# Performance work log

Measured on AMD Instinct MI355X. Metric: run time of the kernel, lower is better.

## Reference

```python
import jax, jax.numpy as jnp
import numpy as np

D_MODEL = 1024
N_HEADS = 16
HEAD_DIM = 64


def setup_inputs() -> dict:
    key = jax.random.key(0)
    ks = jax.random.split(key, 9)
    B, T, C = 4, 2048, D_MODEL
    s = 1.0 / np.sqrt(C)
    return {
        "x": jax.random.normal(ks[0], (B, T, C), jnp.float32),
        "wq": jax.random.normal(ks[1], (C, C), jnp.float32) * s,
        "bq": jnp.zeros((C,), jnp.float32),
        "wk": jax.random.normal(ks[2], (C, C), jnp.float32) * s,
        "bk": jnp.zeros((C,), jnp.float32),
        "wv": jax.random.normal(ks[3], (C, C), jnp.float32) * s,
        "bv": jnp.zeros((C,), jnp.float32),
        "wo": jax.random.normal(ks[4], (C, C), jnp.float32) * s,
        "bo": jnp.zeros((C,), jnp.float32),
    }


def reference(x, wq, bq, wk, bk, wv, bv, wo, bo):
    B, T, C = x.shape
    H, Dh = N_HEADS, HEAD_DIM
    # projections -> (B, H, T, Dh)
    def split_heads(t):
        return t.reshape(B, T, H, Dh).transpose(0, 2, 1, 3)
    q = split_heads(x @ wq + bq)
    k = split_heads(x @ wk + bk)
    v = split_heads(x @ wv + bv)
    scale = 1.0 / jnp.sqrt(jnp.asarray(Dh, x.dtype))
    scores = jnp.einsum("bhqd,bhkd->bhqk", q, k) * scale  # (B,H,T,T)
    causal = jnp.tril(jnp.ones((T, T), bool))
    scores = jnp.where(causal, scores, jnp.asarray(-jnp.inf, x.dtype))
    attn = jax.nn.softmax(scores, axis=-1)
    out = jnp.einsum("bhqk,bhkd->bhqd", attn, v)
    out = out.transpose(0, 2, 1, 3).reshape(B, T, C)
    return out @ wo + bo
```

## Files before the change

kernel.cpp:

```cpp
#include <hip/hip_runtime.h>
#include <hip/hip_bf16.h>
#include <stdint.h>

#define D_MODEL 1024
#define NHEADS 16
#define HDIM 64
#define BATCH 4
#define SEQ 2048
#define M_ROWS (BATCH*SEQ)
#define BHTD ((size_t)BATCH*NHEADS*SEQ*HDIM)

typedef __attribute__((ext_vector_type(8))) short bf16x8;
typedef __attribute__((ext_vector_type(4))) float f32x4;
typedef __attribute__((ext_vector_type(16))) float f32x16;
typedef __attribute__((address_space(1))) uint32_t as1_u32;
typedef __attribute__((address_space(3))) uint32_t as3_u32;

__device__ __forceinline__ void gload_lds16(const void* g, void* l) {
    __builtin_amdgcn_global_load_lds((const as1_u32*)(uintptr_t)g,
                                     (as3_u32*)(uintptr_t)l, 16, 0, 0);
}

__device__ __forceinline__ short f2bf(float f) {
    __hip_bfloat16 h = __float2bfloat16(f);
    return *reinterpret_cast<short*>(&h);
}

__device__ __forceinline__ uint32_t cvtpk_bf16(float lo, float hi) {
    uint32_t r;
    asm("v_cvt_pk_bf16_f32 %0, %1, %2" : "=v"(r) : "v"(lo), "v"(hi));
    return r;
}

__device__ __forceinline__ float fexp2(float x) {
    return __builtin_amdgcn_exp2f(x);
}

__global__ void f32_to_bf16_k(const float* __restrict__ in, short* __restrict__ out, int n) {
    int i = (blockIdx.x * blockDim.x + threadIdx.x) * 4;
    if (i >= n) return;
    float4 v = *(const float4*)&in[i];
    short4 r;
    r.x = f2bf(v.x); r.y = f2bf(v.y); r.z = f2bf(v.z); r.w = f2bf(v.w);
    *(short4*)&out[i] = r;
}

__global__ void transpose_pack_k(const float* __restrict__ wq, const float* __restrict__ wk,
                                 const float* __restrict__ wv, const float* __restrict__ wo,
                                 short* __restrict__ qkvT, short* __restrict__ woT) {
    __shared__ float tile[32][33];
    int z = blockIdx.z;
    const float* src = (z == 0) ? wq : (z == 1) ? wk : (z == 2) ? wv : wo;
    short* dst = (z < 3) ? (qkvT + (size_t)z * D_MODEL * D_MODEL) : woT;
    int bx = blockIdx.x, by = blockIdx.y;
    int tx = threadIdx.x, ty = threadIdx.y;
#pragma unroll
    for (int r = 0; r < 32; r += 8)
        tile[ty + r][tx] = src[(size_t)(by * 32 + ty + r) * D_MODEL + bx * 32 + tx];
    __syncthreads();
#pragma unroll
    for (int r = 0; r < 32; r += 8)
        dst[(size_t)(bx * 32 + ty + r) * D_MODEL + by * 32 + tx] = f2bf(tile[tx][ty + r]);
}

template <int MODE>
__global__ __launch_bounds__(256, 2) void gemm128(const short* __restrict__ A,
                                                  const short* __restrict__ Bt,
                                                  const float* __restrict__ b0,
                                                  const float* __restrict__ b1,
                                                  const float* __restrict__ b2,
                                                  short* __restrict__ outb,
                                                  float* __restrict__ outf,
                                                  int K) {
    __shared__ short As[2][128 * 64];
    __shared__ short Bs[2][128 * 64];
    int tid = threadIdx.x;
    int lane = tid & 63, wid = tid >> 6;
    int wr = wid >> 1, wc = wid & 1;
    int lr = lane & 15, lg = lane >> 4;
    int mb = blockIdx.x * 128;
    int nb = blockIdx.y * 128;
    int srow = tid >> 3, kseg = tid & 7;

    f32x4 acc[4][4] = {};
    int nk = K / 64;

    auto STAGE = [&](int bufi, int kb) {
#pragma unroll
        for (int si = 0; si < 4; ++si) {
            int row = srow + si * 32;
            int sp = kseg ^ (row & 7);
            gload_lds16(A + (size_t)(mb + row) * K + kb + sp * 8, &As[bufi][row * 64 + kseg * 8]);
            gload_lds16(Bt + (size_t)(nb + row) * K + kb + sp * 8, &Bs[bufi][row * 64 + kseg * 8]);
        }
    };

    STAGE(0, 0);
    for (int kt = 0; kt < nk; ++kt) {
        int buf = kt & 1;
        if (kt + 1 < nk) {
            STAGE(buf ^ 1, (kt + 1) * 64);
            asm volatile("s_waitcnt vmcnt(8)" ::: "memory");
        } else {
            asm volatile("s_waitcnt vmcnt(0)" ::: "memory");
        }
        __builtin_amdgcn_s_barrier();
        __builtin_amdgcn_sched_barrier(0);
        bf16x8 af[4][2], bfv[4][2];
#pragma unroll
        for (int ms = 0; ms < 4; ++ms) {
            int row = wr * 64 + ms * 16 + lr;
            int rs = row & 7;
            const short* base = &As[buf][row * 64];
            af[ms][0] = *(const bf16x8*)&base[(lg ^ rs) << 3];
            af[ms][1] = *(const bf16x8*)&base[((4 + lg) ^ rs) << 3];
        }
#pragma unroll
        for (int ns = 0; ns < 4; ++ns) {
            int row = wc * 64 + ns * 16 + lr;
            int rs = row & 7;
            const short* base = &Bs[buf][row * 64];
            bfv[ns][0] = *(const bf16x8*)&base[(lg ^ rs) << 3];
            bfv[ns][1] = *(const bf16x8*)&base[((4 + lg) ^ rs) << 3];
        }
        asm volatile("s_waitcnt lgkmcnt(0)" ::: "memory");
        __builtin_amdgcn_sched_barrier(0);
        __builtin_amdgcn_s_barrier();
        __builtin_amdgcn_sched_barrier(0);
        __builtin_amdgcn_s_setprio(1);
#pragma unroll
        for (int ms = 0; ms < 4; ++ms)
#pragma unroll
            for (int ns = 0; ns < 4; ++ns) {
                acc[ms][ns] = __builtin_amdgcn_mfma_f32_16x16x32_bf16(af[ms][0], bfv[ns][0], acc[ms][ns], 0, 0, 0);
                acc[ms][ns] = __builtin_amdgcn_mfma_f32_16x16x32_bf16(af[ms][1], bfv[ns][1], acc[ms][ns], 0, 0, 0);
            }
        __builtin_amdgcn_s_setprio(0);
    }
#pragma unroll
    for (int ms = 0; ms < 4; ++ms) {
        int row0 = mb + wr * 64 + ms * 16 + lg * 4;
#pragma unroll
        for (int ns = 0; ns < 4; ++ns) {
            int col = nb + wc * 64 + ns * 16 + lr;
            if (MODE == 0) {
                int sec = col >> 10;
                int nn = col & 1023;
                float bias = (sec == 0) ? b0[nn] : (sec == 1) ? b1[nn] : b2[nn];
                int h = nn >> 6, d = nn & 63;
                if (sec == 2) {
                    int bb = row0 >> 11, t0 = row0 & 2047;
                    short4 pk;
#pragma unroll
                    for (int j = 0; j < 4; ++j)
                        *(((short*)&pk) + j) = f2bf(acc[ms][ns][j] + bias);
                    *(short4*)&outb[2 * BHTD + (((size_t)(bb * NHEADS + h)) * HDIM + d) * SEQ + t0] = pk;
                } else {
#pragma unroll
                    for (int j = 0; j < 4; ++j) {
                        int m = row0 + j;
                        int bb = m >> 11, t = m & 2047;
                        float v = acc[ms][ns][j] + bias;
                        if (sec == 0) v *= 0.18033689f;
                        outb[(size_t)sec * BHTD + (((size_t)(bb * NHEADS + h)) * SEQ + t) * HDIM + d] = f2bf(v);
                    }
                }
            } else {
                float bias = b0[col];
#pragma unroll
                for (int j = 0; j < 4; ++j)
                    outf[(size_t)(row0 + j) * D_MODEL + col] = acc[ms][ns][j] + bias;
            }
        }
    }
}

__global__ __launch_bounds__(256, 4) void attn_kernel(const short* __restrict__ Q,
                                                      const short* __restrict__ Kb,
                                                      const short* __restrict__ VTg,
                                                      short* __restrict__ attn_out) {
    __shared__ short Ks[2][4096];
    __shared__ short Vt[2][4096];
    int tid = threadIdx.x, lane = tid & 63, w = tid >> 6;
    int l31 = lane & 31, hi = lane >> 5;

    int linear = blockIdx.x + 8 * blockIdx.y;
    int bh = 8 * (linear & 7) + ((linear >> 3) & 7);
    int qt = 15 - (linear >> 6);
    int b = bh >> 4, h = bh & 15;
    const short* Qp  = Q   + (size_t)bh * SEQ * HDIM;
    const short* Kp  = Kb  + (size_t)bh * SEQ * HDIM;
    const short* VTp = VTg + (size_t)bh * HDIM * SEQ;

    int srow = tid >> 3;
    int kseg = tid & 7;
    int sp   = kseg ^ (srow & 7);
    int swl  = (l31 & 7) << 3;

    int qbase = qt << 7;
    int qrow0 = qbase + w * 32;
    int myq = qrow0 + l31;

    bf16x8 qf[4];
#pragma unroll
    for (int ks = 0; ks < 4; ++ks)
        qf[ks] = *(const bf16x8*)&Qp[(size_t)myq * HDIM + ks * 16 + hi * 8];

    f32x16 o0 = {}, o1 = {};
    float lsum = 0.f;

    int nkb = 2 * qt + 2;
    int buf = 0;
#pragma unroll
    for (int si = 0; si < 2; ++si) {
        int row = srow + si * 32;
        gload_lds16(Kp + (size_t)row * HDIM + sp * 8, &Ks[buf][row * 64 + kseg * 8]);
        gload_lds16(VTp + (size_t)row * SEQ + sp * 8, &Vt[buf][row * 64 + kseg * 8]);
    }
    for (int kvb = 0; kvb < nkb; ++kvb) {
        int tb = kvb << 6;
        __syncthreads();
        if (kvb + 1 < nkb) {
            int tb2 = tb + 64, bn = buf ^ 1;
#pragma unroll
            for (int si = 0; si < 2; ++si) {
                int row = srow + si * 32;
                gload_lds16(Kp + (size_t)(tb2 + row) * HDIM + sp * 8, &Ks[bn][row * 64 + kseg * 8]);
                gload_lds16(VTp + (size_t)row * SEQ + tb2 + sp * 8, &Vt[bn][row * 64 + kseg * 8]);
            }
        }
        int dq = qrow0 - tb;
        if (dq >= 0) {
            bool has1 = dq >= 32;
            const short* ksb = &Ks[buf][0];
            const short* vtb = &Vt[buf][0];
            f32x16 s0 = {}, s1 = {};
            __builtin_amdgcn_s_setprio(1);
#pragma unroll
            for (int ks = 0; ks < 4; ++ks) {
                bf16x8 kf = *(const bf16x8*)&ksb[l31 * 64 + ((ks * 16 + hi * 8) ^ swl)];
                s0 = __builtin_amdgcn_mfma_f32_32x32x16_bf16(kf, qf[ks], s0, 0, 0, 0);
            }
            if (has1) {
#pragma unroll
                for (int ks = 0; ks < 4; ++ks) {
                    bf16x8 kf = *(const bf16x8*)&ksb[(32 + l31) * 64 + ((ks * 16 + hi * 8) ^ swl)];
                    s1 = __builtin_amdgcn_mfma_f32_32x32x16_bf16(kf, qf[ks], s1, 0, 0, 0);
                }
            }
            __builtin_amdgcn_s_setprio(0);
            if (dq == 0) {
                int thr = l31 - 4 * hi;
#pragma unroll
                for (int r = 0; r < 16; ++r) {
                    int crow = (r & 3) + 8 * (r >> 2);
                    s0[r] = (crow > thr) ? -3e38f : s0[r];
                }
            } else if (dq == 32) {
                int thr = l31 - 4 * hi;
#pragma unroll
                for (int r = 0; r < 16; ++r) {
                    int crow = (r & 3) + 8 * (r >> 2);
                    s1[r] = (crow > thr) ? -3e38f : s1[r];
                }
            }
#pragma unroll
            for (int r = 0; r < 16; ++r) s0[r] = fexp2(s0[r]);
            if (has1) {
#pragma unroll
                for (int r = 0; r < 16; ++r) s1[r] = fexp2(s1[r]);
            }
            float pa0, pa1, pa2, pa3;
            pa0 = s0[0] + s0[4]; pa1 = s0[1] + s0[5];
            pa2 = s0[2] + s0[6]; pa3 = s0[3] + s0[7];
            pa0 += s0[8] + s0[12]; pa1 += s0[9] + s0[13];
            pa2 += s0[10] + s0[14]; pa3 += s0[11] + s0[15];
            if (has1) {
                pa0 += s1[0] + s1[4]; pa1 += s1[1] + s1[5];
                pa2 += s1[2] + s1[6]; pa3 += s1[3] + s1[7];
                pa0 += s1[8] + s1[12]; pa1 += s1[9] + s1[13];
                pa2 += s1[10] + s1[14]; pa3 += s1[11] + s1[15];
            }
            float ps = (pa0 + pa1) + (pa2 + pa3);
            ps += __shfl_xor(ps, 32);
            lsum += ps;
            uint32_t W0[8], W1[8];
#pragma unroll
            for (int u = 0; u < 8; ++u) W0[u] = cvtpk_bf16(s0[2 * u], s0[2 * u + 1]);
            if (has1) {
#pragma unroll
                for (int u = 0; u < 8; ++u) W1[u] = cvtpk_bf16(s1[2 * u], s1[2 * u + 1]);
            }
            uint32_t g0[4], g1[4];
#pragma unroll
            for (int ab = 0; ab < 4; ++ab) {
                int ap = ab >> 1, bb = ab & 1;
                uint32_t swv = hi ? W0[4 * ap + bb] : W0[4 * ap + 2 + bb];
                g0[ab] = __shfl_xor(swv, 32);
            }
            if (has1) {
#pragma unroll
                for (int ab = 0; ab < 4; ++ab) {
                    int ap = ab >> 1, bb = ab & 1;
                    uint32_t swv = hi ? W1[4 * ap + bb] : W1[4 * ap + 2 + bb];
                    g1[ab] = __shfl_xor(swv, 32);
                }
            }
            union { uint32_t u[4]; bf16x8 v; } pa[4];
#pragma unroll
            for (int ks = 0; ks < 4; ++ks) {
                const uint32_t* W = (ks < 2) ? W0 : W1;
                const uint32_t* g = (ks < 2) ? g0 : g1;
                int ap = ks & 1;
                pa[ks].u[0] = hi ? g[ap * 2 + 0] : W[4 * ap + 0];
                pa[ks].u[1] = hi ? g[ap * 2 + 1] : W[4 * ap + 1];
                pa[ks].u[2] = hi ? W[4 * ap + 2] : g[ap * 2 + 0];
                pa[ks].u[3] = hi ? W[4 * ap + 3] : g[ap * 2 + 1];
            }
            __builtin_amdgcn_s_setprio(1);
#pragma unroll
            for (int ks = 0; ks < 4; ++ks) {
                if (ks < 2 || has1) {
                    bf16x8 vf0 = *(const bf16x8*)&vtb[l31 * 64 + ((ks * 16 + hi * 8) ^ swl)];
                    o0 = __builtin_amdgcn_mfma_f32_32x32x16_bf16(vf0, pa[ks].v, o0, 0, 0, 0);
                    bf16x8 vf1 = *(const bf16x8*)&vtb[(32 + l31) * 64 + ((ks * 16 + hi * 8) ^ swl)];
                    o1 = __builtin_amdgcn_mfma_f32_32x32x16_bf16(vf1, pa[ks].v, o1, 0, 0, 0);
                }
            }
            __builtin_amdgcn_s_setprio(0);
        }
        buf ^= 1;
    }
    float inv = 1.0f / lsum;
    short* outp = &attn_out[((size_t)(b * SEQ) + myq) * D_MODEL + h * HDIM + 4 * hi];
#pragma unroll
    for (int rq = 0; rq < 4; ++rq) {
        uint32_t a0 = cvtpk_bf16(o0[4 * rq + 0] * inv, o0[4 * rq + 1] * inv);
        uint32_t a1 = cvtpk_bf16(o0[4 * rq + 2] * inv, o0[4 * rq + 3] * inv);
        uint2 pk0 = {a0, a1};
        *(uint2*)(outp + 8 * rq) = pk0;
        uint32_t b0_ = cvtpk_bf16(o1[4 * rq + 0] * inv, o1[4 * rq + 1] * inv);
        uint32_t b1_ = cvtpk_bf16(o1[4 * rq + 2] * inv, o1[4 * rq + 3] * inv);
        uint2 pk1 = {b0_, b1_};
        *(uint2*)(outp + 32 + 8 * rq) = pk1;
    }
}

extern "C" void kernel_launch(void* const* d_in, const int* in_sizes, int n_in,
                              void* d_out, int out_size, void* d_ws, size_t ws_size,
                              hipStream_t stream) {
    const float* x  = (const float*)d_in[0];
    const float* wq = (const float*)d_in[1];
    const float* bq = (const float*)d_in[2];
    const float* wk = (const float*)d_in[3];
    const float* bk = (const float*)d_in[4];
    const float* wv = (const float*)d_in[5];
    const float* bv = (const float*)d_in[6];
    const float* wo = (const float*)d_in[7];
    const float* bo = (const float*)d_in[8];
    float* out = (float*)d_out;

    char* ws = (char*)d_ws;
    size_t off = 0;
    auto alloc = [&](size_t bytes) {
        void* p = ws + off;
        off += (bytes + 255) & ~(size_t)255;
        return p;
    };
    short* xb   = (short*)alloc((size_t)M_ROWS * D_MODEL * 2);
    short* qkvT = (short*)alloc((size_t)3 * D_MODEL * D_MODEL * 2);
    short* woT  = (short*)alloc((size_t)D_MODEL * D_MODEL * 2);
    short* qkv  = (short*)alloc((size_t)3 * BHTD * 2);
    short* ao   = (short*)alloc((size_t)M_ROWS * D_MODEL * 2);

    f32_to_bf16_k<<<dim3(M_ROWS * D_MODEL / (256 * 4)), dim3(256), 0, stream>>>(
        x, xb, M_ROWS * D_MODEL);
    transpose_pack_k<<<dim3(32, 32, 4), dim3(32, 8), 0, stream>>>(wq, wk, wv, wo, qkvT, woT);
    gemm128<0><<<dim3(M_ROWS / 128, 3 * D_MODEL / 128), dim3(256), 0, stream>>>(
        xb, qkvT, bq, bk, bv, qkv, nullptr, D_MODEL);
    attn_kernel<<<dim3(8, 128), dim3(256), 0, stream>>>(
        qkv, qkv + BHTD, qkv + 2 * BHTD, ao);
    gemm128<1><<<dim3(M_ROWS / 128, D_MODEL / 128), dim3(256), 0, stream>>>(
        ao, woT, bo, nullptr, nullptr, nullptr, out, D_MODEL);
}
```

Measured before the change: 150.2 us.

## Fuse prep kernels, split GEMM LDS reads, and enlarge attention query tile

Three separate changes. The activation cast and the weight transpose kernels are merged into one launch. The GEMM inner loop issues the two K-halves of LDS fragment reads in separate phases and starts the first half of the MFMAs under a partial lgkmcnt wait, so LDS latency overlaps with compute. The attention kernel goes to 512 threads and 256-row query tiles with half the grid, so each K/V block loaded into shared memory serves twice as many queries, at the cost of coarser causal load balance and higher per-block resource use.

Measured after the change: 150.8 us. No clear change (+0.4%).

```diff
diff --git a/kernel.cpp b/kernel.cpp
--- a/kernel.cpp
+++ b/kernel.cpp
@@ -36,31 +36,37 @@
     return __builtin_amdgcn_exp2f(x);
 }
 
-__global__ void f32_to_bf16_k(const float* __restrict__ in, short* __restrict__ out, int n) {
-    int i = (blockIdx.x * blockDim.x + threadIdx.x) * 4;
-    if (i >= n) return;
-    float4 v = *(const float4*)&in[i];
-    short4 r;
-    r.x = f2bf(v.x); r.y = f2bf(v.y); r.z = f2bf(v.z); r.w = f2bf(v.w);
-    *(short4*)&out[i] = r;
-}
-
-__global__ void transpose_pack_k(const float* __restrict__ wq, const float* __restrict__ wk,
-                                 const float* __restrict__ wv, const float* __restrict__ wo,
-                                 short* __restrict__ qkvT, short* __restrict__ woT) {
+__global__ __launch_bounds__(256) void prep_k(const float* __restrict__ x,
+                                              const float* __restrict__ wq,
+                                              const float* __restrict__ wk,
+                                              const float* __restrict__ wv,
+                                              const float* __restrict__ wo,
+                                              short* __restrict__ xb,
+                                              short* __restrict__ qkvT,
+                                              short* __restrict__ woT) {
     __shared__ float tile[32][33];
-    int z = blockIdx.z;
-    const float* src = (z == 0) ? wq : (z == 1) ? wk : (z == 2) ? wv : wo;
-    short* dst = (z < 3) ? (qkvT + (size_t)z * D_MODEL * D_MODEL) : woT;
-    int bx = blockIdx.x, by = blockIdx.y;
-    int tx = threadIdx.x, ty = threadIdx.y;
-#pragma unroll
-    for (int r = 0; r < 32; r += 8)
-        tile[ty + r][tx] = src[(size_t)(by * 32 + ty + r) * D_MODEL + bx * 32 + tx];
-    __syncthreads();
-#pragma unroll
-    for (int r = 0; r < 32; r += 8)
-        dst[(size_t)(bx * 32 + ty + r) * D_MODEL + by * 32 + tx] = f2bf(tile[tx][ty + r]);
+    int tid = threadIdx.x;
+    int bid = blockIdx.x;
+    if (bid < 8192) {
+        int i = (bid * 256 + tid) * 4;
+        float4 v = *(const float4*)&x[i];
+        short4 r;
+        r.x = f2bf(v.x); r.y = f2bf(v.y); r.z = f2bf(v.z); r.w = f2bf(v.w);
+        *(short4*)&xb[i] = r;
+    } else {
+        int b2 = bid - 8192;
+        int bx = b2 & 31, by = (b2 >> 5) & 31, z = b2 >> 10;
+        const float* src = (z == 0) ? wq : (z == 1) ? wk : (z == 2) ? wv : wo;
+        short* dst = (z < 3) ? (qkvT + (size_t)z * D_MODEL * D_MODEL) : woT;
+        int tx = tid & 31, ty = tid >> 5;
+#pragma unroll
+        for (int r = 0; r < 32; r += 8)
+            tile[ty + r][tx] = src[(size_t)(by * 32 + ty + r) * D_MODEL + bx * 32 + tx];
+        __syncthreads();
+#pragma unroll
+        for (int r = 0; r < 32; r += 8)
+            dst[(size_t)(bx * 32 + ty + r) * D_MODEL + by * 32 + tx] = f2bf(tile[tx][ty + r]);
+    }
 }
 
 template <int MODE>
@@ -110,19 +116,34 @@
 #pragma unroll
         for (int ms = 0; ms < 4; ++ms) {
             int row = wr * 64 + ms * 16 + lr;
-            int rs = row & 7;
-            const short* base = &As[buf][row * 64];
-            af[ms][0] = *(const bf16x8*)&base[(lg ^ rs) << 3];
-            af[ms][1] = *(const bf16x8*)&base[((4 + lg) ^ rs) << 3];
+            af[ms][0] = *(const bf16x8*)&As[buf][row * 64 + ((lg ^ (row & 7)) << 3)];
         }
 #pragma unroll
         for (int ns = 0; ns < 4; ++ns) {
             int row = wc * 64 + ns * 16 + lr;
-            int rs = row & 7;
-            const short* base = &Bs[buf][row * 64];
-            bfv[ns][0] = *(const bf16x8*)&base[(lg ^ rs) << 3];
-            bfv[ns][1] = *(const bf16x8*)&base[((4 + lg) ^ rs) << 3];
-        }
+            bfv[ns][0] = *(const bf16x8*)&Bs[buf][row * 64 + ((lg ^ (row & 7)) << 3)];
+        }
+        __builtin_amdgcn_sched_barrier(0);
+#pragma unroll
+        for (int ms = 0; ms < 4; ++ms) {
+            int row = wr * 64 + ms * 16 + lr;
+            af[ms][1] = *(const bf16x8*)&As[buf][row * 64 + (((4 + lg) ^ (row & 7)) << 3)];
+        }
+#pragma unroll
+        for (int ns = 0; ns < 4; ++ns) {
+            int row = wc * 64 + ns * 16 + lr;
+            bfv[ns][1] = *(const bf16x8*)&Bs[buf][row * 64 + (((4 + lg) ^ (row & 7)) << 3)];
+        }
+        __builtin_amdgcn_sched_barrier(0);
+        asm volatile("s_waitcnt lgkmcnt(8)" ::: "memory");
+        __builtin_amdgcn_sched_barrier(0);
+        __builtin_amdgcn_s_setprio(1);
+#pragma unroll
+        for (int ms = 0; ms < 4; ++ms)
+#pragma unroll
+            for (int ns = 0; ns < 4; ++ns)
+                acc[ms][ns] = __builtin_amdgcn_mfma_f32_16x16x32_bf16(af[ms][0], bfv[ns][0], acc[ms][ns], 0, 0, 0);
+        __builtin_amdgcn_s_setprio(0);
         asm volatile("s_waitcnt lgkmcnt(0)" ::: "memory");
         __builtin_amdgcn_sched_barrier(0);
         __builtin_amdgcn_s_barrier();
@@ -131,10 +152,8 @@
 #pragma unroll
         for (int ms = 0; ms < 4; ++ms)
 #pragma unroll
-            for (int ns = 0; ns < 4; ++ns) {
-                acc[ms][ns] = __builtin_amdgcn_mfma_f32_16x16x32_bf16(af[ms][0], bfv[ns][0], acc[ms][ns], 0, 0, 0);
+            for (int ns = 0; ns < 4; ++ns)
                 acc[ms][ns] = __builtin_amdgcn_mfma_f32_16x16x32_bf16(af[ms][1], bfv[ns][1], acc[ms][ns], 0, 0, 0);
-            }
         __builtin_amdgcn_s_setprio(0);
     }
 #pragma unroll
@@ -175,7 +194,7 @@
     }
 }
 
-__global__ __launch_bounds__(256, 4) void attn_kernel(const short* __restrict__ Q,
+__global__ __launch_bounds__(512, 4) void attn_kernel(const short* __restrict__ Q,
                                                       const short* __restrict__ Kb,
                                                       const short* __restrict__ VTg,
                                                       short* __restrict__ attn_out) {
@@ -186,7 +205,7 @@
 
     int linear = blockIdx.x + 8 * blockIdx.y;
     int bh = 8 * (linear & 7) + ((linear >> 3) & 7);
-    int qt = 15 - (linear >> 6);
+    int qt = 7 - (linear >> 6);
     int b = bh >> 4, h = bh & 15;
     const short* Qp  = Q   + (size_t)bh * SEQ * HDIM;
     const short* Kp  = Kb  + (size_t)bh * SEQ * HDIM;
@@ -197,7 +216,7 @@
     int sp   = kseg ^ (srow & 7);
     int swl  = (l31 & 7) << 3;
 
-    int qbase = qt << 7;
+    int qbase = qt << 8;
     int qrow0 = qbase + w * 32;
     int myq = qrow0 + l31;
 
@@ -209,25 +228,17 @@
     f32x16 o0 = {}, o1 = {};
     float lsum = 0.f;
 
-    int nkb = 2 * qt + 2;
+    int nkb = 4 * qt + 4;
     int buf = 0;
-#pragma unroll
-    for (int si = 0; si < 2; ++si) {
-        int row = srow + si * 32;
-        gload_lds16(Kp + (size_t)row * HDIM + sp * 8, &Ks[buf][row * 64 + kseg * 8]);
-        gload_lds16(VTp + (size_t)row * SEQ + sp * 8, &Vt[buf][row * 64 + kseg * 8]);
-    }
+    gload_lds16(Kp + (size_t)srow * HDIM + sp * 8, &Ks[buf][srow * 64 + kseg * 8]);
+    gload_lds16(VTp + (size_t)srow * SEQ + sp * 8, &Vt[buf][srow * 64 + kseg * 8]);
     for (int kvb = 0; kvb < nkb; ++kvb) {
         int tb = kvb << 6;
         __syncthreads();
         if (kvb + 1 < nkb) {
             int tb2 = tb + 64, bn = buf ^ 1;
-#pragma unroll
-            for (int si = 0; si < 2; ++si) {
-                int row = srow + si * 32;
-                gload_lds16(Kp + (size_t)(tb2 + row) * HDIM + sp * 8, &Ks[bn][row * 64 + kseg * 8]);
-                gload_lds16(VTp + (size_t)row * SEQ + tb2 + sp * 8, &Vt[bn][row * 64 + kseg * 8]);
-            }
+            gload_lds16(Kp + (size_t)(tb2 + srow) * HDIM + sp * 8, &Ks[bn][srow * 64 + kseg * 8]);
+            gload_lds16(VTp + (size_t)srow * SEQ + tb2 + sp * 8, &Vt[bn][srow * 64 + kseg * 8]);
         }
         int dq = qrow0 - tb;
         if (dq >= 0) {
@@ -373,12 +384,11 @@
     short* qkv  = (short*)alloc((size_t)3 * BHTD * 2);
     short* ao   = (short*)alloc((size_t)M_ROWS * D_MODEL * 2);
 
-    f32_to_bf16_k<<<dim3(M_ROWS * D_MODEL / (256 * 4)), dim3(256), 0, stream>>>(
-        x, xb, M_ROWS * D_MODEL);
-    transpose_pack_k<<<dim3(32, 32, 4), dim3(32, 8), 0, stream>>>(wq, wk, wv, wo, qkvT, woT);
+    prep_k<<<dim3(8192 + 4096), dim3(256), 0, stream>>>(
+        x, wq, wk, wv, wo, xb, qkvT, woT);
     gemm128<0><<<dim3(M_ROWS / 128, 3 * D_MODEL / 128), dim3(256), 0, stream>>>(
         xb, qkvT, bq, bk, bv, qkv, nullptr, D_MODEL);
-    attn_kernel<<<dim3(8, 128), dim3(256), 0, stream>>>(
+    attn_kernel<<<dim3(8, 64), dim3(512), 0, stream>>>(
         qkv, qkv + BHTD, qkv + 2 * BHTD, ao);
     gemm128<1><<<dim3(M_ROWS / 128, D_MODEL / 128), dim3(256), 0, stream>>>(
         ao, woT, bo, nullptr, nullptr, nullptr, out, D_MODEL);
```
